# Kernel optimization log

Measured on AMD Instinct MI355X. Metric: run time of the kernel, lower is better.

Reference implementation:

```python
import jax, jax.numpy as jnp
import numpy as np
import math

N_NEURONS = 2048
MAX_MEMORY = 32
BATCH = 128

def setup_inputs() -> dict:
    key = jax.random.key(0)
    k1, k2, k3 = jax.random.split(key, 3)
    state_trace = jax.random.normal(k1, (BATCH, N_NEURONS, MAX_MEMORY), dtype=jnp.float32)
    fc1_weight = jax.random.normal(k2, (N_NEURONS, MAX_MEMORY, 256), dtype=jnp.float32) * math.sqrt(2.0 / MAX_MEMORY)
    fc1_bias = jnp.zeros((N_NEURONS, 256), dtype=jnp.float32)
    fc2_weight = jax.random.normal(k3, (N_NEURONS, 128, 2), dtype=jnp.float32) * math.sqrt(2.0 / 128)
    fc2_bias = jnp.zeros((N_NEURONS, 2), dtype=jnp.float32)
    T = jnp.ones((1,), dtype=jnp.float32)
    return {"state_trace": state_trace, "fc1_weight": fc1_weight, "fc1_bias": fc1_bias,
            "fc2_weight": fc2_weight, "fc2_bias": fc2_bias, "T": T}

def _glu(x):
    # torch F.glu(dim=-1): first half * sigmoid(second half)
    a, b = jnp.split(x, 2, axis=-1)
    return a * jax.nn.sigmoid(b)

def reference(state_trace, fc1_weight, fc1_bias, fc2_weight, fc2_bias, T):
    # per-neuron batched GEMM 1: (b,n,m) x (n,m,256) -> (b,n,256)
    x_fc1 = jnp.einsum('bnm,nmh->bnh', state_trace, fc1_weight) + fc1_bias
    x_glu1 = _glu(x_fc1)                                   # (b, n, 128)
    # per-neuron batched GEMM 2: (b,n,128) x (n,128,2) -> (b,n,2)
    x_fc2 = jnp.einsum('bnh,nho->bno', x_glu1, fc2_weight) + fc2_bias
    x_glu2 = _glu(x_fc2)                                   # (b, n, 1)
    return jnp.squeeze(x_glu2, -1) / T                     # (b, n)
```

## Files before the change

kernel.cpp:

```cpp
#include <hip/hip_runtime.h>
#include <hip/hip_bf16.h>


#define NN 2048

typedef __attribute__((ext_vector_type(8))) short short8;
typedef __attribute__((ext_vector_type(4))) float floatx4;
typedef __attribute__((ext_vector_type(4))) int int4v;

static __device__ __forceinline__ unsigned int pkbf(float a, float b) {
    __hip_bfloat162 h = __float22bfloat162_rn(make_float2(a, b));
    return *(unsigned int*)&h;
}

static __device__ __forceinline__ float sigmoidf_(float x) {
    return __builtin_amdgcn_rcpf(1.0f + __expf(-x));
}

__global__ __launch_bounds__(256)
void st_transpose_kernel(const float* __restrict__ st, short* __restrict__ st_t)
{
    const int t    = threadIdx.x;
    const int lane = t & 63;
    const int wv   = t >> 6;
    const int mt   = blockIdx.x & 7;
    const int g    = blockIdx.x >> 3;
    const int m    = lane & 15;
    const int quad = lane >> 4;

    const int b = mt * 16 + m;
    const float* src = st + (size_t)b * (NN * 32) + (size_t)quad * 8;
    short* dstbase = st_t + (size_t)mt * 512 + (size_t)lane * 8;

    const int n0 = g * 32 + wv;
    #pragma unroll
    for (int i = 0; i < 8; ++i) {
        const int n = n0 + i * 4;
        floatx4 a0 = *(const floatx4*)(src + (size_t)n * 32);
        floatx4 a1 = *(const floatx4*)(src + (size_t)n * 32 + 4);
        union { int4v iv; short8 s; } u;
        u.iv[0] = pkbf(a0[0], a0[1]);
        u.iv[1] = pkbf(a0[2], a0[3]);
        u.iv[2] = pkbf(a1[0], a1[1]);
        u.iv[3] = pkbf(a1[2], a1[3]);
        *(short8*)(dstbase + (size_t)n * 4096) = u.s;
    }
}

__global__ __launch_bounds__(512, 2)
void nlm_kernel(const short* __restrict__ st_t,
                const float* __restrict__ w1,
                const float* __restrict__ b1,
                const float* __restrict__ w2,
                const float* __restrict__ b2,
                const float* __restrict__ Tp,
                float* __restrict__ out_t)
{
    const int n = blockIdx.x;
    const int t = threadIdx.x;

    __shared__ __align__(16) short ldsB[8192];
    __shared__ float4 ldsP[128];
    __shared__ float  ldsO[128];

    const int lane = t & 63;
    const int wv   = t >> 6;
    const int m    = lane & 15;
    const int quad = lane >> 4;

    short8 afrag = *(const short8*)(st_t + (size_t)n * 4096 + wv * 512 + lane * 8);

    if (t < 128) {
        const float* b1p = b1 + (size_t)n * 256;
        const float* w2p = w2 + (size_t)n * 256;
        float  pba = b1p[t];
        float  pbb = b1p[128 + t];
        float2 pw2 = *(const float2*)(w2p + 2 * t);
        ldsP[t] = make_float4(pba, pbb, pw2.x, pw2.y);
    }
    const float bb0  = b2[n * 2 + 0];
    const float bb1  = b2[n * 2 + 1];
    const float invT = 1.0f / Tp[0];

    {
        const int h  = t & 255;
        const int kh = t >> 8;
        const float* gW = w1 + (size_t)n * 8192 + (size_t)kh * 16 * 256 + h;
        float wr[16];
        #pragma unroll
        for (int j = 0; j < 16; ++j)
            wr[j] = gW[(size_t)j * 256];

        const int base = ((h >> 4) * 512) + ((h & 15) * 8) + kh * 256;
        #pragma unroll
        for (int q = 0; q < 2; ++q) {
            union { int4v iv; short8 s; } u;
            #pragma unroll
            for (int e = 0; e < 4; ++e)
                u.iv[e] = pkbf(wr[q * 8 + 2 * e], wr[q * 8 + 2 * e + 1]);
            *(short8*)&ldsB[base + q * 128] = u.s;
        }
    }

    __syncthreads();

    float pacc[4][2];
    #pragma unroll
    for (int r = 0; r < 4; ++r)
        pacc[r][0] = pacc[r][1] = 0.0f;

    #pragma unroll
    for (int p = 0; p < 8; ++p) {
        short8 bfA = *(short8*)&ldsB[(p * 64 + lane) * 8];
        short8 bfB = *(short8*)&ldsB[((p + 8) * 64 + lane) * 8];
        float4 prm = ldsP[p * 16 + m];
        floatx4 ca = {prm.x, prm.x, prm.x, prm.x};
        floatx4 cb = {prm.y, prm.y, prm.y, prm.y};
        floatx4 xa = __builtin_amdgcn_mfma_f32_16x16x32_bf16(afrag, bfA, ca, 0, 0, 0);
        floatx4 xb = __builtin_amdgcn_mfma_f32_16x16x32_bf16(afrag, bfB, cb, 0, 0, 0);
        #pragma unroll
        for (int r = 0; r < 4; ++r) {
            float glu = xa[r] * sigmoidf_(xb[r]);
            pacc[r][0] += glu * prm.z;
            pacc[r][1] += glu * prm.w;
        }
    }

    #pragma unroll
    for (int r = 0; r < 4; ++r) {
        float s0 = pacc[r][0];
        float s1 = pacc[r][1];
        s0 += __shfl_xor(s0, 1);  s1 += __shfl_xor(s1, 1);
        s0 += __shfl_xor(s0, 2);  s1 += __shfl_xor(s1, 2);
        s0 += __shfl_xor(s0, 4);  s1 += __shfl_xor(s1, 4);
        s0 += __shfl_xor(s0, 8);  s1 += __shfl_xor(s1, 8);
        if (m == 0) {
            const int b = wv * 16 + quad * 4 + r;
            float x0 = s0 + bb0;
            float x1 = s1 + bb1;
            ldsO[b] = x0 * sigmoidf_(x1) * invT;
        }
    }

    __syncthreads();

    if (t < 128)
        out_t[(size_t)n * 128 + t] = ldsO[t];
}

__global__ __launch_bounds__(256)
void transpose_kernel(const float* __restrict__ out_t, float* __restrict__ out)
{
    __shared__ float tile[32][33];
    const int t    = threadIdx.x;
    const int bidx = blockIdx.x;
    const int n0   = (bidx & 63) * 32;
    const int b0   = (bidx >> 6) * 32;

    const int tx = t & 31;
    const int ty = t >> 5;

    #pragma unroll
    for (int i = 0; i < 4; ++i) {
        const int nl = ty + i * 8;
        tile[nl][tx] = out_t[(size_t)(n0 + nl) * 128 + b0 + tx];
    }

    __syncthreads();

    #pragma unroll
    for (int i = 0; i < 4; ++i) {
        const int bl = ty + i * 8;
        out[(size_t)(b0 + bl) * NN + n0 + tx] = tile[tx][bl];
    }
}

extern "C" void kernel_launch(void* const* d_in, const int* in_sizes, int n_in,
                              void* d_out, int out_size, void* d_ws, size_t ws_size,
                              hipStream_t stream) {
    const float* st = (const float*)d_in[0];
    const float* w1 = (const float*)d_in[1];
    const float* b1 = (const float*)d_in[2];
    const float* w2 = (const float*)d_in[3];
    const float* b2 = (const float*)d_in[4];
    const float* T  = (const float*)d_in[5];
    float* out   = (float*)d_out;
    float* out_t = (float*)d_ws;
    short* st_t  = (short*)((char*)d_ws + (2u << 20));

    st_transpose_kernel<<<dim3(512), dim3(256), 0, stream>>>(st, st_t);
    nlm_kernel<<<dim3(NN), dim3(512), 0, stream>>>(st_t, w1, b1, w2, b2, T, out_t);
    transpose_kernel<<<dim3(256), dim3(256), 0, stream>>>(out_t, out);
}
```

Measured before the change: 140.5 us.

## Pre-convert fc1 weights to bf16 MFMA layout in prep kernel, single-wave main kernel

Weight conversion to bf16 and reordering into the MFMA B-fragment layout moves into the prep kernel, which now also performs the state transpose. The main kernel runs one 64-thread wave per neuron. It keeps all 16 weight fragments in registers and loops over the 8 batch tiles, prefetching the next A fragment each iteration. This removes the LDS staging of weights and halves the weight bytes read by the main kernel, at the cost of an extra full write and read of the converted weights in workspace and much smaller blocks with less parallelism per neuron.

```diff
diff --git a/kernel.cpp b/kernel.cpp
--- a/kernel.cpp
+++ b/kernel.cpp
@@ -18,134 +18,150 @@
 }
 
 __global__ __launch_bounds__(256)
-void st_transpose_kernel(const float* __restrict__ st, short* __restrict__ st_t)
+void prep_kernel(const float* __restrict__ st, short* __restrict__ st_t,
+                 const float* __restrict__ w1, short* __restrict__ w1t)
 {
-    const int t    = threadIdx.x;
-    const int lane = t & 63;
-    const int wv   = t >> 6;
-    const int mt   = blockIdx.x & 7;
-    const int g    = blockIdx.x >> 3;
-    const int m    = lane & 15;
-    const int quad = lane >> 4;
-
-    const int b = mt * 16 + m;
-    const float* src = st + (size_t)b * (NN * 32) + (size_t)quad * 8;
-    short* dstbase = st_t + (size_t)mt * 512 + (size_t)lane * 8;
-
-    const int n0 = g * 32 + wv;
-    #pragma unroll
-    for (int i = 0; i < 8; ++i) {
-        const int n = n0 + i * 4;
-        floatx4 a0 = *(const floatx4*)(src + (size_t)n * 32);
-        floatx4 a1 = *(const floatx4*)(src + (size_t)n * 32 + 4);
-        union { int4v iv; short8 s; } u;
-        u.iv[0] = pkbf(a0[0], a0[1]);
-        u.iv[1] = pkbf(a0[2], a0[3]);
-        u.iv[2] = pkbf(a1[0], a1[1]);
-        u.iv[3] = pkbf(a1[2], a1[3]);
-        *(short8*)(dstbase + (size_t)n * 4096) = u.s;
-    }
-}
-
-__global__ __launch_bounds__(512, 2)
+    const int bid = blockIdx.x;
+    const int t   = threadIdx.x;
+
+    if (bid < 512) {
+        const int lane = t & 63;
+        const int wv   = t >> 6;
+        const int mt   = bid & 7;
+        const int g    = bid >> 3;
+        const int m    = lane & 15;
+        const int quad = lane >> 4;
+
+        const int b = mt * 16 + m;
+        const float* src = st + (size_t)b * (NN * 32) + (size_t)quad * 8;
+        short* dstbase = st_t + (size_t)mt * 512 + (size_t)lane * 8;
+
+        const int n0 = g * 32 + wv;
+        #pragma unroll
+        for (int i = 0; i < 8; ++i) {
+            const int n = n0 + i * 4;
+            floatx4 a0 = *(const floatx4*)(src + (size_t)n * 32);
+            floatx4 a1 = *(const floatx4*)(src + (size_t)n * 32 + 4);
+            union { int4v iv; short8 s; } u;
+            u.iv[0] = pkbf(a0[0], a0[1]);
+            u.iv[1] = pkbf(a0[2], a0[3]);
+            u.iv[2] = pkbf(a1[0], a1[1]);
+            u.iv[3] = pkbf(a1[2], a1[3]);
+            *(short8*)(dstbase + (size_t)n * 4096) = u.s;
+        }
+    } else {
+        const int n = bid - 512;
+        const int h = t;
+        const float* gW = w1 + (size_t)n * 8192 + h;
+        float wr[32];
+        #pragma unroll
+        for (int k = 0; k < 32; ++k)
+            wr[k] = gW[(size_t)k * 256];
+
+        short* dst = w1t + (size_t)n * 8192 + ((h >> 4) * 512) + ((h & 15) * 8);
+        #pragma unroll
+        for (int q = 0; q < 4; ++q) {
+            union { int4v iv; short8 s; } u;
+            #pragma unroll
+            for (int e = 0; e < 4; ++e)
+                u.iv[e] = pkbf(wr[q * 8 + 2 * e], wr[q * 8 + 2 * e + 1]);
+            *(short8*)(dst + q * 128) = u.s;
+        }
+    }
+}
+
+__global__ __launch_bounds__(64, 2)
 void nlm_kernel(const short* __restrict__ st_t,
-                const float* __restrict__ w1,
+                const short* __restrict__ w1t,
                 const float* __restrict__ b1,
                 const float* __restrict__ w2,
                 const float* __restrict__ b2,
                 const float* __restrict__ Tp,
                 float* __restrict__ out_t)
 {
-    const int n = blockIdx.x;
-    const int t = threadIdx.x;
-
-    __shared__ __align__(16) short ldsB[8192];
+    const int n    = blockIdx.x;
+    const int lane = threadIdx.x;
+    const int m    = lane & 15;
+    const int quad = lane >> 4;
+
     __shared__ float4 ldsP[128];
     __shared__ float  ldsO[128];
 
-    const int lane = t & 63;
-    const int wv   = t >> 6;
-    const int m    = lane & 15;
-    const int quad = lane >> 4;
-
-    short8 afrag = *(const short8*)(st_t + (size_t)n * 4096 + wv * 512 + lane * 8);
-
-    if (t < 128) {
+    {
         const float* b1p = b1 + (size_t)n * 256;
         const float* w2p = w2 + (size_t)n * 256;
-        float  pba = b1p[t];
-        float  pbb = b1p[128 + t];
-        float2 pw2 = *(const float2*)(w2p + 2 * t);
-        ldsP[t] = make_float4(pba, pbb, pw2.x, pw2.y);
+        #pragma unroll
+        for (int j = 0; j < 2; ++j) {
+            const int hh = lane + 64 * j;
+            ldsP[hh] = make_float4(b1p[hh], b1p[128 + hh],
+                                   w2p[2 * hh], w2p[2 * hh + 1]);
+        }
     }
     const float bb0  = b2[n * 2 + 0];
     const float bb1  = b2[n * 2 + 1];
     const float invT = 1.0f / Tp[0];
 
+    short8 wf[16];
     {
-        const int h  = t & 255;
-        const int kh = t >> 8;
-        const float* gW = w1 + (size_t)n * 8192 + (size_t)kh * 16 * 256 + h;
-        float wr[16];
-        #pragma unroll
-        for (int j = 0; j < 16; ++j)
-            wr[j] = gW[(size_t)j * 256];
-
-        const int base = ((h >> 4) * 512) + ((h & 15) * 8) + kh * 256;
-        #pragma unroll
-        for (int q = 0; q < 2; ++q) {
-            union { int4v iv; short8 s; } u;
+        const short* gw = w1t + (size_t)n * 8192 + (size_t)lane * 8;
+        #pragma unroll
+        for (int p = 0; p < 16; ++p)
+            wf[p] = *(const short8*)(gw + p * 512);
+    }
+
+    __syncthreads();
+
+    const short* ga = st_t + (size_t)n * 4096 + (size_t)lane * 8;
+    short8 acur = *(const short8*)ga;
+
+    #pragma unroll 1
+    for (int mt = 0; mt < 8; ++mt) {
+        short8 anext = acur;
+        if (mt < 7) anext = *(const short8*)(ga + (mt + 1) * 512);
+
+        float pacc[4][2];
+        #pragma unroll
+        for (int r = 0; r < 4; ++r)
+            pacc[r][0] = pacc[r][1] = 0.0f;
+
+        #pragma unroll
+        for (int p = 0; p < 8; ++p) {
+            float4 prm = ldsP[p * 16 + m];
+            floatx4 ca = {prm.x, prm.x, prm.x, prm.x};
+            floatx4 cb = {prm.y, prm.y, prm.y, prm.y};
+            floatx4 xa = __builtin_amdgcn_mfma_f32_16x16x32_bf16(acur, wf[p],     ca, 0, 0, 0);
+            floatx4 xb = __builtin_amdgcn_mfma_f32_16x16x32_bf16(acur, wf[p + 8], cb, 0, 0, 0);
             #pragma unroll
-            for (int e = 0; e < 4; ++e)
-                u.iv[e] = pkbf(wr[q * 8 + 2 * e], wr[q * 8 + 2 * e + 1]);
-            *(short8*)&ldsB[base + q * 128] = u.s;
-        }
+            for (int r = 0; r < 4; ++r) {
+                float glu = xa[r] * sigmoidf_(xb[r]);
+                pacc[r][0] += glu * prm.z;
+                pacc[r][1] += glu * prm.w;
+            }
+        }
+
+        #pragma unroll
+        for (int r = 0; r < 4; ++r) {
+            float s0 = pacc[r][0];
+            float s1 = pacc[r][1];
+            s0 += __shfl_xor(s0, 1);  s1 += __shfl_xor(s1, 1);
+            s0 += __shfl_xor(s0, 2);  s1 += __shfl_xor(s1, 2);
+            s0 += __shfl_xor(s0, 4);  s1 += __shfl_xor(s1, 4);
+            s0 += __shfl_xor(s0, 8);  s1 += __shfl_xor(s1, 8);
+            if (m == 0) {
+                const int b = mt * 16 + quad * 4 + r;
+                float x0 = s0 + bb0;
+                float x1 = s1 + bb1;
+                ldsO[b] = x0 * sigmoidf_(x1) * invT;
+            }
+        }
+
+        acur = anext;
     }
 
     __syncthreads();
 
-    float pacc[4][2];
-    #pragma unroll
-    for (int r = 0; r < 4; ++r)
-        pacc[r][0] = pacc[r][1] = 0.0f;
-
-    #pragma unroll
-    for (int p = 0; p < 8; ++p) {
-        short8 bfA = *(short8*)&ldsB[(p * 64 + lane) * 8];
-        short8 bfB = *(short8*)&ldsB[((p + 8) * 64 + lane) * 8];
-        float4 prm = ldsP[p * 16 + m];
-        floatx4 ca = {prm.x, prm.x, prm.x, prm.x};
-        floatx4 cb = {prm.y, prm.y, prm.y, prm.y};
-        floatx4 xa = __builtin_amdgcn_mfma_f32_16x16x32_bf16(afrag, bfA, ca, 0, 0, 0);
-        floatx4 xb = __builtin_amdgcn_mfma_f32_16x16x32_bf16(afrag, bfB, cb, 0, 0, 0);
-        #pragma unroll
-        for (int r = 0; r < 4; ++r) {
-            float glu = xa[r] * sigmoidf_(xb[r]);
-            pacc[r][0] += glu * prm.z;
-            pacc[r][1] += glu * prm.w;
-        }
-    }
-
-    #pragma unroll
-    for (int r = 0; r < 4; ++r) {
-        float s0 = pacc[r][0];
-        float s1 = pacc[r][1];
-        s0 += __shfl_xor(s0, 1);  s1 += __shfl_xor(s1, 1);
-        s0 += __shfl_xor(s0, 2);  s1 += __shfl_xor(s1, 2);
-        s0 += __shfl_xor(s0, 4);  s1 += __shfl_xor(s1, 4);
-        s0 += __shfl_xor(s0, 8);  s1 += __shfl_xor(s1, 8);
-        if (m == 0) {
-            const int b = wv * 16 + quad * 4 + r;
-            float x0 = s0 + bb0;
-            float x1 = s1 + bb1;
-            ldsO[b] = x0 * sigmoidf_(x1) * invT;
-        }
-    }
-
-    __syncthreads();
-
-    if (t < 128)
-        out_t[(size_t)n * 128 + t] = ldsO[t];
+    out_t[(size_t)n * 128 + lane]      = ldsO[lane];
+    out_t[(size_t)n * 128 + 64 + lane] = ldsO[64 + lane];
 }
 
 __global__ __launch_bounds__(256)
@@ -186,9 +202,10 @@
     const float* T  = (const float*)d_in[5];
     float* out   = (float*)d_out;
     float* out_t = (float*)d_ws;
-    short* st_t  = (short*)((char*)d_ws + (2u << 20));
-
-    st_transpose_kernel<<<dim3(512), dim3(256), 0, stream>>>(st, st_t);
-    nlm_kernel<<<dim3(NN), dim3(512), 0, stream>>>(st_t, w1, b1, w2, b2, T, out_t);
+    short* st_t  = (short*)((char*)d_ws + (2u  << 20));
+    short* w1t   = (short*)((char*)d_ws + (32u << 20));
+
+    prep_kernel<<<dim3(2560), dim3(256), 0, stream>>>(st, st_t, w1, w1t);
+    nlm_kernel<<<dim3(NN), dim3(64), 0, stream>>>(st_t, w1t, b1, w2, b2, T, out_t);
     transpose_kernel<<<dim3(256), dim3(256), 0, stream>>>(out_t, out);
 }
```

Measured after the change: 157.5 us. 1.12x slower.
